# Performance work log

Hardware: AMD Instinct MI355X
Metric: run time of the kernel (lower is better)

The kernel has to match this reference:

```python
import jax, jax.numpy as jnp
import numpy as np

ETA = 0.01
EPSILON = 1e-08


def setup_inputs() -> dict:
    key = jax.random.key(0)
    k1, k2 = jax.random.split(key)
    B, N = 2000000, 16  # batch (time steps), num_assets
    weights = jax.random.uniform(k1, (B, N), dtype=jnp.float32)
    next_returns = jax.random.normal(k2, (B, N), dtype=jnp.float32) * 0.02
    return {"weights": weights, "next_returns": next_returns}


def reference(weights, next_returns):
    # portfolio return per time step: (B,)
    R = jnp.sum(weights * next_returns, axis=1)
    batch_size = R.shape[0]
    eta = jnp.asarray(ETA, R.dtype)
    eps = jnp.asarray(EPSILON, R.dtype)

    def step(carry, R_t):
        A_prev, B_prev = carry
        delta_A = eta * (R_t - A_prev)
        delta_B = eta * (R_t * R_t - B_prev)
        variance = jnp.maximum(B_prev - A_prev * A_prev, eps)
        denom = variance ** 1.5
        D_t = (B_prev * delta_A - 0.5 * A_prev * delta_B) / denom
        return (A_prev + delta_A, B_prev + delta_B), D_t

    init = (jnp.asarray(0.0, R.dtype), jnp.asarray(EPSILON, R.dtype))
    _, D = jax.lax.scan(step, init, R)
    return -jnp.sum(D) / batch_size
```

## Files before the change

### kernel.cpp

```cpp
#include <hip/hip_runtime.h>


#define D_ETA 0.01
#define D_C   (1.0 - D_ETA)
#define D_EPS 1e-8

constexpr int BLOCK  = 256;
constexpr int CHUNK  = 1024;
constexpr int LPT    = CHUNK / BLOCK;
constexpr int PASSES = CHUNK / 64;

typedef float f32x4 __attribute__((ext_vector_type(4)));

__device__ __forceinline__ void block_scan(double& m, double& sA, double& sB,
                                           double* mS, double* aS, double* bS) {
    int tid = threadIdx.x;
    mS[tid] = m; aS[tid] = sA; bS[tid] = sB;
    __syncthreads();
#pragma unroll
    for (int off = 1; off < BLOCK; off <<= 1) {
        double pm = 1.0, pa = 0.0, pb = 0.0;
        if (tid >= off) { pm = mS[tid - off]; pa = aS[tid - off]; pb = bS[tid - off]; }
        __syncthreads();
        if (tid >= off) {
            sA = m * pa + sA;
            sB = m * pb + sB;
            m  = pm * m;
        }
        mS[tid] = m; aS[tid] = sA; bS[tid] = sB;
        __syncthreads();
    }
}

__global__ __launch_bounds__(BLOCK, 6) void k1_fused(
    const float* __restrict__ w, const float* __restrict__ x, int nrows,
    float* __restrict__ Rws,
    double* __restrict__ blkM, double* __restrict__ blkA, double* __restrict__ blkB)
{
    __shared__ double Qs[2][CHUNK];
    __shared__ double mS[BLOCK], aS[BLOCK], bS[BLOCK];

    const int tid = threadIdx.x;
    const int b   = blockIdx.x;
    const long long base = (long long)b * CHUNK;
    const int q    = tid & 3;
    const int rsub = tid >> 2;
    const f32x4* w4 = (const f32x4*)w;
    const f32x4* x4 = (const f32x4*)x;

    const bool full = (base + CHUNK <= (long long)nrows);

    if (full) {
        const long long f0 = base * 4 + tid;
        f32x4 a0 = __builtin_nontemporal_load(&w4[f0]);
        f32x4 c0 = __builtin_nontemporal_load(&x4[f0]);
        f32x4 a1 = __builtin_nontemporal_load(&w4[f0 + 256]);
        f32x4 c1 = __builtin_nontemporal_load(&x4[f0 + 256]);
        f32x4 a2 = __builtin_nontemporal_load(&w4[f0 + 512]);
        f32x4 c2 = __builtin_nontemporal_load(&x4[f0 + 512]);
        f32x4 a3 = __builtin_nontemporal_load(&w4[f0 + 768]);
        f32x4 c3 = __builtin_nontemporal_load(&x4[f0 + 768]);
#pragma unroll
        for (int p = 0; p < PASSES; ++p) {
            f32x4 an = (f32x4)(0.f);
            f32x4 cn = (f32x4)(0.f);
            if (p + 4 < PASSES) {
                an = __builtin_nontemporal_load(&w4[f0 + (long long)(p + 4) * 256]);
                cn = __builtin_nontemporal_load(&x4[f0 + (long long)(p + 4) * 256]);
            }
            __builtin_amdgcn_sched_barrier(0);
            double d = (double)a0.x * c0.x + (double)a0.y * c0.y
                     + (double)a0.z * c0.z + (double)a0.w * c0.w;
            d += __shfl_xor(d, 1, 64);
            if ((q & 1) == 0)
                Qs[q >> 1][p * 64 + rsub] = d;
            a0 = a1; c0 = c1;
            a1 = a2; c1 = c2;
            a2 = a3; c2 = c3;
            a3 = an; c3 = cn;
        }
    } else {
        for (int p = 0; p < PASSES; ++p) {
            long long row = base + (long long)p * 64 + rsub;
            double d = 0.0;
            if (row < (long long)nrows) {
                long long f = row * 4 + q;
                f32x4 a = w4[f], c = x4[f];
                d = (double)a.x * c.x + (double)a.y * c.y
                  + (double)a.z * c.z + (double)a.w * c.w;
            }
            d += __shfl_xor(d, 1, 64);
            if ((q & 1) == 0 && row < (long long)nrows)
                Qs[q >> 1][p * 64 + rsub] = d;
        }
    }
    __syncthreads();

    long long g0 = base + (long long)tid * LPT;
    long long rem = (long long)nrows - g0;
    int len = rem >= LPT ? LPT : (rem > 0 ? (int)rem : 0);

    float rv[LPT];
#pragma unroll
    for (int r = 0; r < LPT; ++r) {
        int lr = tid * LPT + r;
        rv[r] = (float)(Qs[0][lr] + Qs[1][lr]);
    }

    if (len == LPT) {
        *(float4*)(Rws + g0) = make_float4(rv[0], rv[1], rv[2], rv[3]);
    } else {
        for (int k = 0; k < len; ++k) Rws[g0 + k] = rv[k];
    }

    double m = 1.0, sA = 0.0, sB = 0.0;
    for (int k = 0; k < len; ++k) {
        double r = (double)rv[k];
        sA = D_C * sA + D_ETA * r;
        sB = D_C * sB + D_ETA * (r * r);
        m *= D_C;
    }
    block_scan(m, sA, sB, mS, aS, bS);
    if (tid == BLOCK - 1) {
        blkM[b] = m;
        blkA[b] = sA;
        blkB[b] = sB;
    }
}

__device__ __forceinline__ float row_R(const float* __restrict__ w,
                                       const float* __restrict__ x,
                                       long long row) {
    const float4* w4 = (const float4*)(w + row * 16);
    const float4* x4 = (const float4*)(x + row * 16);
    double d0, d1, d2, d3;
    {
        float4 a = w4[0], b = x4[0];
        d0 = (double)a.x * b.x + (double)a.y * b.y
           + (double)a.z * b.z + (double)a.w * b.w;
    }
    {
        float4 a = w4[1], b = x4[1];
        d1 = (double)a.x * b.x + (double)a.y * b.y
           + (double)a.z * b.z + (double)a.w * b.w;
    }
    {
        float4 a = w4[2], b = x4[2];
        d2 = (double)a.x * b.x + (double)a.y * b.y
           + (double)a.z * b.z + (double)a.w * b.w;
    }
    {
        float4 a = w4[3], b = x4[3];
        d3 = (double)a.x * b.x + (double)a.y * b.y
           + (double)a.z * b.z + (double)a.w * b.w;
    }
    return (float)((d0 + d1) + (d2 + d3));
}

__device__ __forceinline__ int load_seg(const float* __restrict__ Rws,
                                        const float* __restrict__ w,
                                        const float* __restrict__ x,
                                        long long g0, int nrows, float* rv) {
    long long rem = (long long)nrows - g0;
    int len = rem >= LPT ? LPT : (rem > 0 ? (int)rem : 0);
    if (Rws) {
        if (len == LPT) {
            f32x4 u = __builtin_nontemporal_load((const f32x4*)(Rws + g0));
            rv[0] = u.x; rv[1] = u.y; rv[2] = u.z; rv[3] = u.w;
        } else {
            for (int k = 0; k < len; ++k) rv[k] = Rws[g0 + k];
        }
    } else {
        for (int k = 0; k < len; ++k) rv[k] = row_R(w, x, g0 + k);
    }
    return len;
}

__global__ __launch_bounds__(BLOCK) void k2_partials(
    const float* __restrict__ Rws,
    const float* __restrict__ w, const float* __restrict__ x, int nrows,
    double* __restrict__ blkM, double* __restrict__ blkA, double* __restrict__ blkB)
{
    __shared__ double mS[BLOCK], aS[BLOCK], bS[BLOCK];
    int tid = threadIdx.x;
    long long g0 = (long long)blockIdx.x * CHUNK + (long long)tid * LPT;
    float rv[LPT];
    int len = load_seg(Rws, w, x, g0, nrows, rv);

    double m = 1.0, sA = 0.0, sB = 0.0;
    for (int k = 0; k < len; ++k) {
        double r = (double)rv[k];
        sA = D_C * sA + D_ETA * r;
        sB = D_C * sB + D_ETA * (r * r);
        m *= D_C;
    }
    block_scan(m, sA, sB, mS, aS, bS);
    if (tid == BLOCK - 1) {
        blkM[blockIdx.x] = m;
        blkA[blockIdx.x] = sA;
        blkB[blockIdx.x] = sB;
    }
}

__global__ __launch_bounds__(BLOCK) void k3_scan(
    int nb,
    const double* __restrict__ blkM, const double* __restrict__ blkA,
    const double* __restrict__ blkB,
    double* __restrict__ A0, double* __restrict__ B0)
{
    __shared__ double mS[BLOCK], aS[BLOCK], bS[BLOCK];
    int tid = threadIdx.x;
    int K = (nb + BLOCK - 1) / BLOCK;
    int g0 = tid * K;
    int g1 = g0 + K; if (g1 > nb) g1 = nb;

    double m = 1.0, sA = 0.0, sB = 0.0;
    for (int g = g0; g < g1; ++g) {
        double mg = blkM[g], ag = blkA[g], bg = blkB[g];
        sA = mg * sA + ag;
        sB = mg * sB + bg;
        m *= mg;
    }
    block_scan(m, sA, sB, mS, aS, bS);

    double em = 1.0, ea = 0.0, eb = 0.0;
    if (tid > 0) { em = mS[tid - 1]; ea = aS[tid - 1]; eb = bS[tid - 1]; }
    double A = ea;
    double B = em * D_EPS + eb;
    for (int g = g0; g < g1; ++g) {
        A0[g] = A; B0[g] = B;
        double mg = blkM[g], ag = blkA[g], bg = blkB[g];
        A = mg * A + ag;
        B = mg * B + bg;
    }
}

__global__ __launch_bounds__(BLOCK) void k4_dsum(
    const float* __restrict__ Rws,
    const float* __restrict__ w, const float* __restrict__ x, int nrows,
    const double* __restrict__ A0, const double* __restrict__ B0,
    double* __restrict__ bsum)
{
    __shared__ double mS[BLOCK], aS[BLOCK], bS[BLOCK];
    __shared__ double wsum[BLOCK / 64];
    int tid = threadIdx.x;
    long long g0 = (long long)blockIdx.x * CHUNK + (long long)tid * LPT;
    float rv[LPT];
    int len = load_seg(Rws, w, x, g0, nrows, rv);

    double m = 1.0, sA = 0.0, sB = 0.0;
    for (int k = 0; k < len; ++k) {
        double r = (double)rv[k];
        sA = D_C * sA + D_ETA * r;
        sB = D_C * sB + D_ETA * (r * r);
        m *= D_C;
    }
    block_scan(m, sA, sB, mS, aS, bS);

    double em = 1.0, ea = 0.0, eb = 0.0;
    if (tid > 0) { em = mS[tid - 1]; ea = aS[tid - 1]; eb = bS[tid - 1]; }
    double A = em * A0[blockIdx.x] + ea;
    double B = em * B0[blockIdx.x] + eb;

    double dsum = 0.0;
    for (int k = 0; k < len; ++k) {
        double r = (double)rv[k];
        double dA = D_ETA * (r - A);
        double dB = D_ETA * (r * r - B);
        double var = B - A * A;
        if (var < D_EPS) var = D_EPS;
        double denom = var * sqrt(var);
        dsum += (B * dA - 0.5 * A * dB) / denom;
        A += dA;
        B += dB;
    }

#pragma unroll
    for (int off = 32; off > 0; off >>= 1) dsum += __shfl_down(dsum, off, 64);
    if ((tid & 63) == 0) wsum[tid >> 6] = dsum;
    __syncthreads();
    if (tid == 0) bsum[blockIdx.x] = wsum[0] + wsum[1] + wsum[2] + wsum[3];
}

__global__ __launch_bounds__(BLOCK) void k5_final(
    const double* __restrict__ bsum, int nb, int nrows, float* __restrict__ out)
{
    __shared__ double sh[BLOCK / 64];
    int tid = threadIdx.x;
    double s = 0.0;
    for (int i = tid; i < nb; i += BLOCK) s += bsum[i];
#pragma unroll
    for (int off = 32; off > 0; off >>= 1) s += __shfl_down(s, off, 64);
    if ((tid & 63) == 0) sh[tid >> 6] = s;
    __syncthreads();
    if (tid == 0) out[0] = (float)(-(sh[0] + sh[1] + sh[2] + sh[3]) / (double)nrows);
}

extern "C" void kernel_launch(void* const* d_in, const int* in_sizes, int n_in,
                              void* d_out, int out_size, void* d_ws, size_t ws_size,
                              hipStream_t stream)
{
    const float* w = (const float*)d_in[0];
    const float* x = (const float*)d_in[1];
    int nrows = in_sizes[0] / 16;
    int nb  = (nrows + CHUNK - 1) / CHUNK;

    char* ws = (char*)d_ws;
    double* blkM = (double*)(ws + 64);
    double* blkA = blkM + nb;
    double* blkB = blkA + nb;
    double* A0   = blkB + nb;
    double* B0   = A0 + nb;
    double* bsum = B0 + nb;

    size_t off = 64 + (size_t)6 * nb * sizeof(double);
    off = (off + 255) & ~(size_t)255;
    float* Rws = nullptr;
    if (ws_size >= off + (size_t)nrows * sizeof(float))
        Rws = (float*)(ws + off);

    if (Rws) {
        k1_fused<<<nb, BLOCK, 0, stream>>>(w, x, nrows, Rws, blkM, blkA, blkB);
    } else {
        k2_partials<<<nb, BLOCK, 0, stream>>>(Rws, w, x, nrows, blkM, blkA, blkB);
    }
    k3_scan<<<1, BLOCK, 0, stream>>>(nb, blkM, blkA, blkB, A0, B0);
    k4_dsum<<<nb, BLOCK, 0, stream>>>(Rws, w, x, nrows, A0, B0, bsum);
    k5_final<<<1, BLOCK, 0, stream>>>(bsum, nb, nrows, (float*)d_out);
}
```

Before: 267.5 us.

## Stage input tiles into LDS via global_load_lds and halve chunk size

Replaces the register-pipelined nontemporal vector loads in the first kernel with direct global-to-LDS async copies of a full weights/returns tile, then computes row dot products from LDS. The chunk per block drops from 1024 to 512 rows, the per-row reduction is finished with a second shuffle and stored as float, and the Rws store/load width shrinks to match. The 64 KB LDS tile lowers the occupancy hint from 6 to 2 blocks per CU, trading latency hiding for bulk async transfer, and doubles the number of blocks and block-level partials for the later scan stages.

Result: slower. 308.3 us (+15.3%).

```diff
diff --git a/kernel.cpp b/kernel.cpp
--- a/kernel.cpp
+++ b/kernel.cpp
@@ -6,11 +6,20 @@
 #define D_EPS 1e-8
 
 constexpr int BLOCK  = 256;
-constexpr int CHUNK  = 1024;
+constexpr int CHUNK  = 512;
 constexpr int LPT    = CHUNK / BLOCK;
 constexpr int PASSES = CHUNK / 64;
+constexpr int LOADS_PER_WAVE = 8;
 
 typedef float f32x4 __attribute__((ext_vector_type(4)));
+typedef float f32x2 __attribute__((ext_vector_type(2)));
+
+__device__ __forceinline__ void glds16(const void* gsrc, void* ldst) {
+    __builtin_amdgcn_global_load_lds(
+        (const __attribute__((address_space(1))) unsigned int*)gsrc,
+        (__attribute__((address_space(3))) unsigned int*)(unsigned long long)ldst,
+        16, 0, 0);
+}
 
 __device__ __forceinline__ void block_scan(double& m, double& sA, double& sB,
                                            double* mS, double* aS, double* bS) {
@@ -32,54 +41,53 @@
     }
 }
 
-__global__ __launch_bounds__(BLOCK, 6) void k1_fused(
+__global__ __launch_bounds__(BLOCK, 2) void k1_fused(
     const float* __restrict__ w, const float* __restrict__ x, int nrows,
     float* __restrict__ Rws,
     double* __restrict__ blkM, double* __restrict__ blkA, double* __restrict__ blkB)
 {
-    __shared__ double Qs[2][CHUNK];
+    __shared__ float  wtile[CHUNK * 16];
+    __shared__ float  xtile[CHUNK * 16];
+    __shared__ float  R_l[CHUNK];
     __shared__ double mS[BLOCK], aS[BLOCK], bS[BLOCK];
 
-    const int tid = threadIdx.x;
-    const int b   = blockIdx.x;
+    const int tid  = threadIdx.x;
+    const int b    = blockIdx.x;
     const long long base = (long long)b * CHUNK;
     const int q    = tid & 3;
     const int rsub = tid >> 2;
-    const f32x4* w4 = (const f32x4*)w;
-    const f32x4* x4 = (const f32x4*)x;
+    const int wv   = tid >> 6;
+    const int lane = tid & 63;
 
     const bool full = (base + CHUNK <= (long long)nrows);
 
     if (full) {
-        const long long f0 = base * 4 + tid;
-        f32x4 a0 = __builtin_nontemporal_load(&w4[f0]);
-        f32x4 c0 = __builtin_nontemporal_load(&x4[f0]);
-        f32x4 a1 = __builtin_nontemporal_load(&w4[f0 + 256]);
-        f32x4 c1 = __builtin_nontemporal_load(&x4[f0 + 256]);
-        f32x4 a2 = __builtin_nontemporal_load(&w4[f0 + 512]);
-        f32x4 c2 = __builtin_nontemporal_load(&x4[f0 + 512]);
-        f32x4 a3 = __builtin_nontemporal_load(&w4[f0 + 768]);
-        f32x4 c3 = __builtin_nontemporal_load(&x4[f0 + 768]);
+        const char* wsrc = (const char*)w + (unsigned long long)base * 64;
+        const char* xsrc = (const char*)x + (unsigned long long)base * 64;
+#pragma unroll
+        for (int i = 0; i < LOADS_PER_WAVE; ++i) {
+            const int L = wv * LOADS_PER_WAVE + i;
+            const unsigned long long goff =
+                (unsigned long long)L * 1024ull + (unsigned long long)lane * 16ull;
+            glds16(wsrc + goff, &wtile[L * 256]);
+            glds16(xsrc + goff, &xtile[L * 256]);
+        }
+        __syncthreads();
+
 #pragma unroll
         for (int p = 0; p < PASSES; ++p) {
-            f32x4 an = (f32x4)(0.f);
-            f32x4 cn = (f32x4)(0.f);
-            if (p + 4 < PASSES) {
-                an = __builtin_nontemporal_load(&w4[f0 + (long long)(p + 4) * 256]);
-                cn = __builtin_nontemporal_load(&x4[f0 + (long long)(p + 4) * 256]);
-            }
-            __builtin_amdgcn_sched_barrier(0);
-            double d = (double)a0.x * c0.x + (double)a0.y * c0.y
-                     + (double)a0.z * c0.z + (double)a0.w * c0.w;
+            const int row = p * 64 + rsub;
+            f32x4 a = *(const f32x4*)&wtile[row * 16 + q * 4];
+            f32x4 c = *(const f32x4*)&xtile[row * 16 + q * 4];
+            double d = (double)a.x * c.x + (double)a.y * c.y
+                     + (double)a.z * c.z + (double)a.w * c.w;
             d += __shfl_xor(d, 1, 64);
-            if ((q & 1) == 0)
-                Qs[q >> 1][p * 64 + rsub] = d;
-            a0 = a1; c0 = c1;
-            a1 = a2; c1 = c2;
-            a2 = a3; c2 = c3;
-            a3 = an; c3 = cn;
+            d += __shfl_xor(d, 2, 64);
+            if (q == 0) R_l[row] = (float)d;
         }
     } else {
+        const f32x4* w4 = (const f32x4*)w;
+        const f32x4* x4 = (const f32x4*)x;
         for (int p = 0; p < PASSES; ++p) {
             long long row = base + (long long)p * 64 + rsub;
             double d = 0.0;
@@ -90,8 +98,8 @@
                   + (double)a.z * c.z + (double)a.w * c.w;
             }
             d += __shfl_xor(d, 1, 64);
-            if ((q & 1) == 0 && row < (long long)nrows)
-                Qs[q >> 1][p * 64 + rsub] = d;
+            d += __shfl_xor(d, 2, 64);
+            if (q == 0 && row < (long long)nrows) R_l[p * 64 + rsub] = (float)d;
         }
     }
     __syncthreads();
@@ -102,13 +110,10 @@
 
     float rv[LPT];
 #pragma unroll
-    for (int r = 0; r < LPT; ++r) {
-        int lr = tid * LPT + r;
-        rv[r] = (float)(Qs[0][lr] + Qs[1][lr]);
-    }
+    for (int r = 0; r < LPT; ++r) rv[r] = R_l[tid * LPT + r];
 
     if (len == LPT) {
-        *(float4*)(Rws + g0) = make_float4(rv[0], rv[1], rv[2], rv[3]);
+        *(f32x2*)(Rws + g0) = (f32x2){rv[0], rv[1]};
     } else {
         for (int k = 0; k < len; ++k) Rws[g0 + k] = rv[k];
     }
@@ -165,8 +170,8 @@
     int len = rem >= LPT ? LPT : (rem > 0 ? (int)rem : 0);
     if (Rws) {
         if (len == LPT) {
-            f32x4 u = __builtin_nontemporal_load((const f32x4*)(Rws + g0));
-            rv[0] = u.x; rv[1] = u.y; rv[2] = u.z; rv[3] = u.w;
+            f32x2 u = __builtin_nontemporal_load((const f32x2*)(Rws + g0));
+            rv[0] = u.x; rv[1] = u.y;
         } else {
             for (int k = 0; k < len; ++k) rv[k] = Rws[g0 + k];
         }
```

## Drop single-block carry scan by recomputing block prefixes inside dsum kernel

Applied to the files above, without the earlier changes.

Removes the single-block k3_scan kernel and the A0/B0 arrays. Each k4_dsum block now recomputes its own starting (A,B) state by scanning the k1 block summaries that precede it. k4 also processes 2048 rows per block, 8 per thread, so each k4 block's prefix spans twice as many k1 blocks. This removes one serial launch and the latency of the one-block scan, but adds redundant O(nb) prefix work in every k4 block, which grows with the block index.

New measurement: 259.5 us. 1.03x faster.

```diff
diff --git a/kernel.cpp b/kernel.cpp
--- a/kernel.cpp
+++ b/kernel.cpp
@@ -5,10 +5,12 @@
 #define D_C   (1.0 - D_ETA)
 #define D_EPS 1e-8
 
-constexpr int BLOCK  = 256;
-constexpr int CHUNK  = 1024;
-constexpr int LPT    = CHUNK / BLOCK;
-constexpr int PASSES = CHUNK / 64;
+constexpr int BLOCK   = 256;
+constexpr int CHUNK1  = 1024;
+constexpr int LPT1    = CHUNK1 / BLOCK;
+constexpr int PASSES  = CHUNK1 / 64;
+constexpr int CHUNK4  = 2048;
+constexpr int LPT4    = CHUNK4 / BLOCK;
 
 typedef float f32x4 __attribute__((ext_vector_type(4)));
 
@@ -37,18 +39,18 @@
     float* __restrict__ Rws,
     double* __restrict__ blkM, double* __restrict__ blkA, double* __restrict__ blkB)
 {
-    __shared__ double Qs[2][CHUNK];
+    __shared__ double Qs[2][CHUNK1];
     __shared__ double mS[BLOCK], aS[BLOCK], bS[BLOCK];
 
     const int tid = threadIdx.x;
     const int b   = blockIdx.x;
-    const long long base = (long long)b * CHUNK;
+    const long long base = (long long)b * CHUNK1;
     const int q    = tid & 3;
     const int rsub = tid >> 2;
     const f32x4* w4 = (const f32x4*)w;
     const f32x4* x4 = (const f32x4*)x;
 
-    const bool full = (base + CHUNK <= (long long)nrows);
+    const bool full = (base + CHUNK1 <= (long long)nrows);
 
     if (full) {
         const long long f0 = base * 4 + tid;
@@ -96,18 +98,18 @@
     }
     __syncthreads();
 
-    long long g0 = base + (long long)tid * LPT;
+    long long g0 = base + (long long)tid * LPT1;
     long long rem = (long long)nrows - g0;
-    int len = rem >= LPT ? LPT : (rem > 0 ? (int)rem : 0);
-
-    float rv[LPT];
-#pragma unroll
-    for (int r = 0; r < LPT; ++r) {
-        int lr = tid * LPT + r;
+    int len = rem >= LPT1 ? LPT1 : (rem > 0 ? (int)rem : 0);
+
+    float rv[LPT1];
+#pragma unroll
+    for (int r = 0; r < LPT1; ++r) {
+        int lr = tid * LPT1 + r;
         rv[r] = (float)(Qs[0][lr] + Qs[1][lr]);
     }
 
-    if (len == LPT) {
+    if (len == LPT1) {
         *(float4*)(Rws + g0) = make_float4(rv[0], rv[1], rv[2], rv[3]);
     } else {
         for (int k = 0; k < len; ++k) Rws[g0 + k] = rv[k];
@@ -157,35 +159,82 @@
     return (float)((d0 + d1) + (d2 + d3));
 }
 
-__device__ __forceinline__ int load_seg(const float* __restrict__ Rws,
-                                        const float* __restrict__ w,
-                                        const float* __restrict__ x,
-                                        long long g0, int nrows, float* rv) {
+__global__ __launch_bounds__(BLOCK) void k2_partials(
+    const float* __restrict__ w, const float* __restrict__ x, int nrows,
+    double* __restrict__ blkM, double* __restrict__ blkA, double* __restrict__ blkB)
+{
+    __shared__ double mS[BLOCK], aS[BLOCK], bS[BLOCK];
+    int tid = threadIdx.x;
+    long long g0 = (long long)blockIdx.x * CHUNK1 + (long long)tid * LPT1;
     long long rem = (long long)nrows - g0;
-    int len = rem >= LPT ? LPT : (rem > 0 ? (int)rem : 0);
+    int len = rem >= LPT1 ? LPT1 : (rem > 0 ? (int)rem : 0);
+
+    double m = 1.0, sA = 0.0, sB = 0.0;
+    for (int k = 0; k < len; ++k) {
+        double r = (double)row_R(w, x, g0 + k);
+        sA = D_C * sA + D_ETA * r;
+        sB = D_C * sB + D_ETA * (r * r);
+        m *= D_C;
+    }
+    block_scan(m, sA, sB, mS, aS, bS);
+    if (tid == BLOCK - 1) {
+        blkM[blockIdx.x] = m;
+        blkA[blockIdx.x] = sA;
+        blkB[blockIdx.x] = sB;
+    }
+}
+
+__global__ __launch_bounds__(BLOCK) void k4_dsum(
+    const float* __restrict__ Rws,
+    const float* __restrict__ w, const float* __restrict__ x, int nrows,
+    const double* __restrict__ blkM, const double* __restrict__ blkA,
+    const double* __restrict__ blkB,
+    double* __restrict__ bsum)
+{
+    __shared__ double mS[BLOCK], aS[BLOCK], bS[BLOCK];
+    __shared__ double wsum[BLOCK / 64];
+    const int tid = threadIdx.x;
+    const int b   = blockIdx.x;
+
+    double Astart, Bstart;
+    {
+        const int H = 2 * b;
+        const int K = (H + BLOCK - 1) / BLOCK;
+        double cm = 1.0, ca = 0.0, cb = 0.0;
+        int s0 = tid * K;
+        int s1 = s0 + K; if (s1 > H) s1 = H;
+        for (int g = s0; g < s1; ++g) {
+            double mg = blkM[g], ag = blkA[g], bg = blkB[g];
+            ca = mg * ca + ag;
+            cb = mg * cb + bg;
+            cm *= mg;
+        }
+        block_scan(cm, ca, cb, mS, aS, bS);
+        double M  = mS[BLOCK - 1];
+        double SA = aS[BLOCK - 1];
+        double SB = bS[BLOCK - 1];
+        Astart = SA;
+        Bstart = M * D_EPS + SB;
+    }
+    __syncthreads();
+
+    long long g0 = (long long)b * CHUNK4 + (long long)tid * LPT4;
+    long long rem = (long long)nrows - g0;
+    int len = rem >= LPT4 ? LPT4 : (rem > 0 ? (int)rem : 0);
+
+    float rv[LPT4];
     if (Rws) {
-        if (len == LPT) {
+        if (len == LPT4) {
             f32x4 u = __builtin_nontemporal_load((const f32x4*)(Rws + g0));
-            rv[0] = u.x; rv[1] = u.y; rv[2] = u.z; rv[3] = u.w;
+            f32x4 v = __builtin_nontemporal_load((const f32x4*)(Rws + g0 + 4));
+            rv[0]=u.x; rv[1]=u.y; rv[2]=u.z; rv[3]=u.w;
+            rv[4]=v.x; rv[5]=v.y; rv[6]=v.z; rv[7]=v.w;
         } else {
             for (int k = 0; k < len; ++k) rv[k] = Rws[g0 + k];
         }
     } else {
         for (int k = 0; k < len; ++k) rv[k] = row_R(w, x, g0 + k);
     }
-    return len;
-}
-
-__global__ __launch_bounds__(BLOCK) void k2_partials(
-    const float* __restrict__ Rws,
-    const float* __restrict__ w, const float* __restrict__ x, int nrows,
-    double* __restrict__ blkM, double* __restrict__ blkA, double* __restrict__ blkB)
-{
-    __shared__ double mS[BLOCK], aS[BLOCK], bS[BLOCK];
-    int tid = threadIdx.x;
-    long long g0 = (long long)blockIdx.x * CHUNK + (long long)tid * LPT;
-    float rv[LPT];
-    int len = load_seg(Rws, w, x, g0, nrows, rv);
 
     double m = 1.0, sA = 0.0, sB = 0.0;
     for (int k = 0; k < len; ++k) {
@@ -195,72 +244,11 @@
         m *= D_C;
     }
     block_scan(m, sA, sB, mS, aS, bS);
-    if (tid == BLOCK - 1) {
-        blkM[blockIdx.x] = m;
-        blkA[blockIdx.x] = sA;
-        blkB[blockIdx.x] = sB;
-    }
-}
-
-__global__ __launch_bounds__(BLOCK) void k3_scan(
-    int nb,
-    const double* __restrict__ blkM, const double* __restrict__ blkA,
-    const double* __restrict__ blkB,
-    double* __restrict__ A0, double* __restrict__ B0)
-{
-    __shared__ double mS[BLOCK], aS[BLOCK], bS[BLOCK];
-    int tid = threadIdx.x;
-    int K = (nb + BLOCK - 1) / BLOCK;
-    int g0 = tid * K;
-    int g1 = g0 + K; if (g1 > nb) g1 = nb;
-
-    double m = 1.0, sA = 0.0, sB = 0.0;
-    for (int g = g0; g < g1; ++g) {
-        double mg = blkM[g], ag = blkA[g], bg = blkB[g];
-        sA = mg * sA + ag;
-        sB = mg * sB + bg;
-        m *= mg;
-    }
-    block_scan(m, sA, sB, mS, aS, bS);
 
     double em = 1.0, ea = 0.0, eb = 0.0;
     if (tid > 0) { em = mS[tid - 1]; ea = aS[tid - 1]; eb = bS[tid - 1]; }
-    double A = ea;
-    double B = em * D_EPS + eb;
-    for (int g = g0; g < g1; ++g) {
-        A0[g] = A; B0[g] = B;
-        double mg = blkM[g], ag = blkA[g], bg = blkB[g];
-        A = mg * A + ag;
-        B = mg * B + bg;
-    }
-}
-
-__global__ __launch_bounds__(BLOCK) void k4_dsum(
-    const float* __restrict__ Rws,
-    const float* __restrict__ w, const float* __restrict__ x, int nrows,
-    const double* __restrict__ A0, const double* __restrict__ B0,
-    double* __restrict__ bsum)
-{
-    __shared__ double mS[BLOCK], aS[BLOCK], bS[BLOCK];
-    __shared__ double wsum[BLOCK / 64];
-    int tid = threadIdx.x;
-    long long g0 = (long long)blockIdx.x * CHUNK + (long long)tid * LPT;
-    float rv[LPT];
-    int len = load_seg(Rws, w, x, g0, nrows, rv);
-
-    double m = 1.0, sA = 0.0, sB = 0.0;
-    for (int k = 0; k < len; ++k) {
-        double r = (double)rv[k];
-        sA = D_C * sA + D_ETA * r;
-        sB = D_C * sB + D_ETA * (r * r);
-        m *= D_C;
-    }
-    block_scan(m, sA, sB, mS, aS, bS);
-
-    double em = 1.0, ea = 0.0, eb = 0.0;
-    if (tid > 0) { em = mS[tid - 1]; ea = aS[tid - 1]; eb = bS[tid - 1]; }
-    double A = em * A0[blockIdx.x] + ea;
-    double B = em * B0[blockIdx.x] + eb;
+    double A = em * Astart + ea;
+    double B = em * Bstart + eb;
 
     double dsum = 0.0;
     for (int k = 0; k < len; ++k) {
@@ -279,7 +267,7 @@
     for (int off = 32; off > 0; off >>= 1) dsum += __shfl_down(dsum, off, 64);
     if ((tid & 63) == 0) wsum[tid >> 6] = dsum;
     __syncthreads();
-    if (tid == 0) bsum[blockIdx.x] = wsum[0] + wsum[1] + wsum[2] + wsum[3];
+    if (tid == 0) bsum[b] = wsum[0] + wsum[1] + wsum[2] + wsum[3];
 }
 
 __global__ __launch_bounds__(BLOCK) void k5_final(
@@ -303,28 +291,26 @@
     const float* w = (const float*)d_in[0];
     const float* x = (const float*)d_in[1];
     int nrows = in_sizes[0] / 16;
-    int nb  = (nrows + CHUNK - 1) / CHUNK;
+    int nb1 = (nrows + CHUNK1 - 1) / CHUNK1;
+    int nb4 = (nrows + CHUNK4 - 1) / CHUNK4;
 
     char* ws = (char*)d_ws;
     double* blkM = (double*)(ws + 64);
-    double* blkA = blkM + nb;
-    double* blkB = blkA + nb;
-    double* A0   = blkB + nb;
-    double* B0   = A0 + nb;
-    double* bsum = B0 + nb;
-
-    size_t off = 64 + (size_t)6 * nb * sizeof(double);
+    double* blkA = blkM + nb1;
+    double* blkB = blkA + nb1;
+    double* bsum = blkB + nb1;
+
+    size_t off = 64 + ((size_t)3 * nb1 + nb4) * sizeof(double);
     off = (off + 255) & ~(size_t)255;
     float* Rws = nullptr;
     if (ws_size >= off + (size_t)nrows * sizeof(float))
         Rws = (float*)(ws + off);
 
     if (Rws) {
-        k1_fused<<<nb, BLOCK, 0, stream>>>(w, x, nrows, Rws, blkM, blkA, blkB);
+        k1_fused<<<nb1, BLOCK, 0, stream>>>(w, x, nrows, Rws, blkM, blkA, blkB);
     } else {
-        k2_partials<<<nb, BLOCK, 0, stream>>>(Rws, w, x, nrows, blkM, blkA, blkB);
-    }
-    k3_scan<<<1, BLOCK, 0, stream>>>(nb, blkM, blkA, blkB, A0, B0);
-    k4_dsum<<<nb, BLOCK, 0, stream>>>(Rws, w, x, nrows, A0, B0, bsum);
-    k5_final<<<1, BLOCK, 0, stream>>>(bsum, nb, nrows, (float*)d_out);
-}
+        k2_partials<<<nb1, BLOCK, 0, stream>>>(w, x, nrows, blkM, blkA, blkB);
+    }
+    k4_dsum<<<nb4, BLOCK, 0, stream>>>(Rws, w, x, nrows, blkM, blkA, blkB, bsum);
+    k5_final<<<1, BLOCK, 0, stream>>>(bsum, nb4, nrows, (float*)d_out);
+}
```
